# Performance work log

Hardware: AMD Instinct MI355X
Metric: run time of the kernel (lower is better)

The kernel has to match this reference:

```python
import jax, jax.numpy as jnp
import numpy as np

N = 1_000_000
F = 64
G = 8          # num_groups
B = 16         # number of point clouds in batch
EPS = 1e-8


def setup_inputs() -> dict:
    key = jax.random.key(0)
    k1, k2 = jax.random.split(key)
    feats = jax.random.normal(k1, (N, F), dtype=jnp.float32)
    batch_ids = jnp.sort(jax.random.randint(k2, (N,), 0, B))
    gamma = jnp.ones((1, F), dtype=jnp.float32)
    beta = jnp.zeros((1, F), dtype=jnp.float32)
    return {"feats": feats, "batch_ids": batch_ids, "gamma": gamma, "beta": beta}


def reference(feats, batch_ids, gamma, beta):
    gs = F // G  # group_size
    # [N, F] -> [N*gs, G]: each row holds one channel-within-group across all groups
    cur = feats.reshape(-1, G)
    ids = jnp.repeat(batch_ids, gs)  # [N*gs]
    counts = jax.ops.segment_sum(jnp.ones_like(ids, dtype=cur.dtype), ids, num_segments=B)
    counts = jnp.maximum(counts, 1.0)[:, None]                # [B, 1]
    means = jax.ops.segment_sum(cur, ids, num_segments=B) / counts   # [B, G]
    m = means[ids]                                            # [N*gs, G]
    var = jax.ops.segment_sum((cur - m) ** 2, ids, num_segments=B) / counts  # [B, G]
    normed = (cur - m) / jnp.sqrt(var[ids] + EPS)             # [N*gs, G]
    out = normed.reshape(-1, F)
    return out * gamma + beta
```

## Files before the change

### kernel.cpp

```cpp
#include <hip/hip_runtime.h>

#define GN_EPS 1e-8f

static constexpr int F    = 64;
static constexpr int G    = 8;
static constexpr int NB   = 16;
static constexpr int BLK  = 256;
static constexpr int GRID = 2048;

typedef float f32x4 __attribute__((ext_vector_type(4)));

__global__ void gn_prep(const int* __restrict__ ids, int n, int* __restrict__ off,
                        float* __restrict__ zbuf ) {
    const int t = threadIdx.x;
    if (t < 2 * NB * G) zbuf[t] = 0.f;
    if (t < NB + 1) {
        int lo = 0, hi = n;
        while (lo < hi) {
            int mid = (lo + hi) >> 1;
            if (ids[mid] < t) lo = mid + 1; else hi = mid;
        }
        off[t] = lo;
    }
}

__global__ __launch_bounds__(BLK) void gn_stats(
        const float* __restrict__ feats, const int* __restrict__ off_g, int n,
        float* __restrict__ gsum, float* __restrict__ gsq) {
    __shared__ float lsum[NB * G];
    __shared__ float lsq [NB * G];
    __shared__ int   soff[NB + 1];
    const int t = threadIdx.x;
    if (t < NB * G) { lsum[t] = 0.f; lsq[t] = 0.f; }
    if (t < NB + 1) soff[t] = off_g[t];
    __syncthreads();

    const int rpb  = (n + GRID - 1) / GRID;
    const int row0 = (int)blockIdx.x * rpb;
    const int row1 = min(n, row0 + rpb);

    if (row0 < row1) {
        const int quad   = t & 15;
        const int subrow = t >> 4;
        const int lane   = t & 63;
        int b = 0, cur = row0;
        while (cur < row1) {
            while (soff[b + 1] <= cur) ++b;
            const int send = min(row1, soff[b + 1]);
            float s0=0.f,s1=0.f,s2=0.f,s3=0.f,q0=0.f,q1=0.f,q2=0.f,q3=0.f;
            const float* p = feats + (size_t)(cur + subrow) * F + quad * 4;
            int base = cur;
            #pragma unroll 2
            for (; base + 32 <= send; base += 32, p += 32 * F) {
                const float4 x0 = *reinterpret_cast<const float4*>(p);
                const float4 x1 = *reinterpret_cast<const float4*>(p + 16 * F);
                s0 += x0.x; q0 = fmaf(x0.x, x0.x, q0);
                s1 += x0.y; q1 = fmaf(x0.y, x0.y, q1);
                s2 += x0.z; q2 = fmaf(x0.z, x0.z, q2);
                s3 += x0.w; q3 = fmaf(x0.w, x0.w, q3);
                s0 += x1.x; q0 = fmaf(x1.x, x1.x, q0);
                s1 += x1.y; q1 = fmaf(x1.y, x1.y, q1);
                s2 += x1.z; q2 = fmaf(x1.z, x1.z, q2);
                s3 += x1.w; q3 = fmaf(x1.w, x1.w, q3);
            }
            if (base + 16 <= send) {
                const float4 x = *reinterpret_cast<const float4*>(p);
                s0 += x.x; q0 = fmaf(x.x, x.x, q0);
                s1 += x.y; q1 = fmaf(x.y, x.y, q1);
                s2 += x.z; q2 = fmaf(x.z, x.z, q2);
                s3 += x.w; q3 = fmaf(x.w, x.w, q3);
                base += 16; p += 16 * F;
            }
            if (base + subrow < send) {
                const float4 x = *reinterpret_cast<const float4*>(p);
                s0 += x.x; q0 = fmaf(x.x, x.x, q0);
                s1 += x.y; q1 = fmaf(x.y, x.y, q1);
                s2 += x.z; q2 = fmaf(x.z, x.z, q2);
                s3 += x.w; q3 = fmaf(x.w, x.w, q3);
            }
            #pragma unroll
            for (int m = 2; m <= 32; m <<= 1) {
                s0 += __shfl_xor(s0, m); s1 += __shfl_xor(s1, m);
                s2 += __shfl_xor(s2, m); s3 += __shfl_xor(s3, m);
                q0 += __shfl_xor(q0, m); q1 += __shfl_xor(q1, m);
                q2 += __shfl_xor(q2, m); q3 += __shfl_xor(q3, m);
            }
            if (lane < 2) {
                float* ps = &lsum[b * G + lane * 4];
                float* pq = &lsq [b * G + lane * 4];
                atomicAdd(ps + 0, s0); atomicAdd(ps + 1, s1);
                atomicAdd(ps + 2, s2); atomicAdd(ps + 3, s3);
                atomicAdd(pq + 0, q0); atomicAdd(pq + 1, q1);
                atomicAdd(pq + 2, q2); atomicAdd(pq + 3, q3);
            }
            cur = send;
        }
    }
    __syncthreads();
    if (t < NB * G) {
        atomicAdd(&gsum[t], lsum[t]);
        atomicAdd(&gsq [t], lsq [t]);
    }
}

__global__ __launch_bounds__(BLK) void gn_norm(
        const float* __restrict__ feats, const int* __restrict__ off_g, int n,
        const float* __restrict__ gsum, const float* __restrict__ gsq,
        const float* __restrict__ gamma, const float* __restrict__ beta,
        float* __restrict__ out) {
    __shared__ int soff[NB + 1];
    const int t = threadIdx.x;
    if (t < NB + 1) soff[t] = off_g[t];
    __syncthreads();

    const int rpb  = (n + GRID - 1) / GRID;
    const int row0 = (int)blockIdx.x * rpb;
    const int row1 = min(n, row0 + rpb);
    if (row0 >= row1) return;

    const int quad   = t & 15;
    const int subrow = t >> 4;
    const float4 gm = *reinterpret_cast<const float4*>(gamma + quad * 4);
    const float4 bt = *reinterpret_cast<const float4*>(beta  + quad * 4);

    int b = 0, cur = row0;
    while (cur < row1) {
        while (soff[b + 1] <= cur) ++b;
        const int send = min(row1, soff[b + 1]);
        const float4 sm = *reinterpret_cast<const float4*>(gsum + b * G + (quad & 1) * 4);
        const float4 sq = *reinterpret_cast<const float4*>(gsq  + b * G + (quad & 1) * 4);
        const float cnt = (float)max((soff[b + 1] - soff[b]) * (F / G), 1);
        const float rc  = 1.0f / cnt;
        f32x4 a, c;
        {
            const float m0 = sm.x * rc, m1 = sm.y * rc, m2 = sm.z * rc, m3 = sm.w * rc;
            const float v0 = fmaxf(sq.x * rc - m0 * m0, 0.f);
            const float v1 = fmaxf(sq.y * rc - m1 * m1, 0.f);
            const float v2 = fmaxf(sq.z * rc - m2 * m2, 0.f);
            const float v3 = fmaxf(sq.w * rc - m3 * m3, 0.f);
            a.x = gm.x / sqrtf(v0 + GN_EPS); a.y = gm.y / sqrtf(v1 + GN_EPS);
            a.z = gm.z / sqrtf(v2 + GN_EPS); a.w = gm.w / sqrtf(v3 + GN_EPS);
            c.x = fmaf(-m0, a.x, bt.x); c.y = fmaf(-m1, a.y, bt.y);
            c.z = fmaf(-m2, a.z, bt.z); c.w = fmaf(-m3, a.w, bt.w);
        }
        const float* p  = feats + (size_t)(cur + subrow) * F + quad * 4;
        float*       po = out   + (size_t)(cur + subrow) * F + quad * 4;
        int base = cur;
        #pragma unroll 2
        for (; base + 32 <= send; base += 32, p += 32 * F, po += 32 * F) {
            const f32x4 x0 = __builtin_nontemporal_load(reinterpret_cast<const f32x4*>(p));
            const f32x4 x1 = __builtin_nontemporal_load(reinterpret_cast<const f32x4*>(p + 16 * F));
            f32x4 o0, o1;
            o0.x = fmaf(x0.x, a.x, c.x); o0.y = fmaf(x0.y, a.y, c.y);
            o0.z = fmaf(x0.z, a.z, c.z); o0.w = fmaf(x0.w, a.w, c.w);
            o1.x = fmaf(x1.x, a.x, c.x); o1.y = fmaf(x1.y, a.y, c.y);
            o1.z = fmaf(x1.z, a.z, c.z); o1.w = fmaf(x1.w, a.w, c.w);
            __builtin_nontemporal_store(o0, reinterpret_cast<f32x4*>(po));
            __builtin_nontemporal_store(o1, reinterpret_cast<f32x4*>(po + 16 * F));
        }
        if (base + 16 <= send) {
            const f32x4 x = __builtin_nontemporal_load(reinterpret_cast<const f32x4*>(p));
            f32x4 o;
            o.x = fmaf(x.x, a.x, c.x); o.y = fmaf(x.y, a.y, c.y);
            o.z = fmaf(x.z, a.z, c.z); o.w = fmaf(x.w, a.w, c.w);
            __builtin_nontemporal_store(o, reinterpret_cast<f32x4*>(po));
            base += 16; p += 16 * F; po += 16 * F;
        }
        if (base + subrow < send) {
            const f32x4 x = __builtin_nontemporal_load(reinterpret_cast<const f32x4*>(p));
            f32x4 o;
            o.x = fmaf(x.x, a.x, c.x); o.y = fmaf(x.y, a.y, c.y);
            o.z = fmaf(x.z, a.z, c.z); o.w = fmaf(x.w, a.w, c.w);
            __builtin_nontemporal_store(o, reinterpret_cast<f32x4*>(po));
        }
        cur = send;
    }
}

extern "C" void kernel_launch(void* const* d_in, const int* in_sizes, int n_in,
                              void* d_out, int out_size, void* d_ws, size_t ws_size,
                              hipStream_t stream) {
    const float* feats = (const float*)d_in[0];
    const int*   ids   = (const int*)  d_in[1];
    const float* gamma = (const float*)d_in[2];
    const float* beta  = (const float*)d_in[3];
    const int n = in_sizes[1];

    float* gsum = (float*)d_ws;
    float* gsq  = gsum + NB * G;
    int*   off  = (int*)(gsq + NB * G);

    gn_prep <<<1, BLK, 0, stream>>>(ids, n, off, gsum);
    gn_stats<<<GRID, BLK, 0, stream>>>(feats, off, n, gsum, gsq);
    gn_norm <<<GRID, BLK, 0, stream>>>(feats, off, n, gsum, gsq, gamma, beta, (float*)d_out);
}
```

Measured before the change: 156.5 us.

## Spread stats atomics over slots and traverse norm rows in reverse order

```diff
diff --git a/kernel.cpp b/kernel.cpp
--- a/kernel.cpp
+++ b/kernel.cpp
@@ -2,18 +2,20 @@
 
 #define GN_EPS 1e-8f
 
-static constexpr int F    = 64;
-static constexpr int G    = 8;
-static constexpr int NB   = 16;
-static constexpr int BLK  = 256;
-static constexpr int GRID = 2048;
+static constexpr int F     = 64;
+static constexpr int G     = 8;
+static constexpr int NB    = 16;
+static constexpr int BLK   = 256;
+static constexpr int GRID  = 2048;
+static constexpr int NSLOT = 16;
 
 typedef float f32x4 __attribute__((ext_vector_type(4)));
+
 
 __global__ void gn_prep(const int* __restrict__ ids, int n, int* __restrict__ off,
                         float* __restrict__ zbuf ) {
     const int t = threadIdx.x;
-    if (t < 2 * NB * G) zbuf[t] = 0.f;
+    for (int i = t; i < 2 * NSLOT * NB * G; i += BLK) zbuf[i] = 0.f;
     if (t < NB + 1) {
         int lo = 0, hi = n;
         while (lo < hi) {
@@ -50,10 +52,11 @@
             float s0=0.f,s1=0.f,s2=0.f,s3=0.f,q0=0.f,q1=0.f,q2=0.f,q3=0.f;
             const float* p = feats + (size_t)(cur + subrow) * F + quad * 4;
             int base = cur;
-            #pragma unroll 2
-            for (; base + 32 <= send; base += 32, p += 32 * F) {
+            for (; base + 64 <= send; base += 64, p += 64 * F) {
                 const float4 x0 = *reinterpret_cast<const float4*>(p);
                 const float4 x1 = *reinterpret_cast<const float4*>(p + 16 * F);
+                const float4 x2 = *reinterpret_cast<const float4*>(p + 32 * F);
+                const float4 x3 = *reinterpret_cast<const float4*>(p + 48 * F);
                 s0 += x0.x; q0 = fmaf(x0.x, x0.x, q0);
                 s1 += x0.y; q1 = fmaf(x0.y, x0.y, q1);
                 s2 += x0.z; q2 = fmaf(x0.z, x0.z, q2);
@@ -62,14 +65,21 @@
                 s1 += x1.y; q1 = fmaf(x1.y, x1.y, q1);
                 s2 += x1.z; q2 = fmaf(x1.z, x1.z, q2);
                 s3 += x1.w; q3 = fmaf(x1.w, x1.w, q3);
-            }
-            if (base + 16 <= send) {
+                s0 += x2.x; q0 = fmaf(x2.x, x2.x, q0);
+                s1 += x2.y; q1 = fmaf(x2.y, x2.y, q1);
+                s2 += x2.z; q2 = fmaf(x2.z, x2.z, q2);
+                s3 += x2.w; q3 = fmaf(x2.w, x2.w, q3);
+                s0 += x3.x; q0 = fmaf(x3.x, x3.x, q0);
+                s1 += x3.y; q1 = fmaf(x3.y, x3.y, q1);
+                s2 += x3.z; q2 = fmaf(x3.z, x3.z, q2);
+                s3 += x3.w; q3 = fmaf(x3.w, x3.w, q3);
+            }
+            for (; base + 16 <= send; base += 16, p += 16 * F) {
                 const float4 x = *reinterpret_cast<const float4*>(p);
                 s0 += x.x; q0 = fmaf(x.x, x.x, q0);
                 s1 += x.y; q1 = fmaf(x.y, x.y, q1);
                 s2 += x.z; q2 = fmaf(x.z, x.z, q2);
                 s3 += x.w; q3 = fmaf(x.w, x.w, q3);
-                base += 16; p += 16 * F;
             }
             if (base + subrow < send) {
                 const float4 x = *reinterpret_cast<const float4*>(p);
@@ -98,8 +108,9 @@
     }
     __syncthreads();
     if (t < NB * G) {
-        atomicAdd(&gsum[t], lsum[t]);
-        atomicAdd(&gsq [t], lsq [t]);
+        const int slot = (int)blockIdx.x & (NSLOT - 1);
+        atomicAdd(&gsum[slot * NB * G + t], lsum[t]);
+        atomicAdd(&gsq [slot * NB * G + t], lsq [t]);
     }
 }
 
@@ -123,12 +134,16 @@
     const float4 gm = *reinterpret_cast<const float4*>(gamma + quad * 4);
     const float4 bt = *reinterpret_cast<const float4*>(beta  + quad * 4);
 
-    int b = 0, cur = row0;
-    while (cur < row1) {
-        while (soff[b + 1] <= cur) ++b;
-        const int send = min(row1, soff[b + 1]);
-        const float4 sm = *reinterpret_cast<const float4*>(gsum + b * G + (quad & 1) * 4);
-        const float4 sq = *reinterpret_cast<const float4*>(gsq  + b * G + (quad & 1) * 4);
+    int b = NB - 1, e = row1;
+    while (e > row0) {
+        while (soff[b] >= e) --b;
+        const int sstart = max(row0, soff[b]);
+        f32x4 sm = {0.f, 0.f, 0.f, 0.f}, sq = {0.f, 0.f, 0.f, 0.f};
+        #pragma unroll
+        for (int k = 0; k < NSLOT; ++k) {
+            sm += *reinterpret_cast<const f32x4*>(gsum + k * NB * G + b * G + (quad & 1) * 4);
+            sq += *reinterpret_cast<const f32x4*>(gsq  + k * NB * G + b * G + (quad & 1) * 4);
+        }
         const float cnt = (float)max((soff[b + 1] - soff[b]) * (F / G), 1);
         const float rc  = 1.0f / cnt;
         f32x4 a, c;
@@ -143,37 +158,47 @@
             c.x = fmaf(-m0, a.x, bt.x); c.y = fmaf(-m1, a.y, bt.y);
             c.z = fmaf(-m2, a.z, bt.z); c.w = fmaf(-m3, a.w, bt.w);
         }
-        const float* p  = feats + (size_t)(cur + subrow) * F + quad * 4;
-        float*       po = out   + (size_t)(cur + subrow) * F + quad * 4;
-        int base = cur;
-        #pragma unroll 2
-        for (; base + 32 <= send; base += 32, p += 32 * F, po += 32 * F) {
+        int hi = e;
+        for (; hi - sstart >= 64; hi -= 64) {
+            const float* p  = feats + (size_t)(hi - 64 + subrow) * F + quad * 4;
+            float*       po = out   + (size_t)(hi - 64 + subrow) * F + quad * 4;
             const f32x4 x0 = __builtin_nontemporal_load(reinterpret_cast<const f32x4*>(p));
             const f32x4 x1 = __builtin_nontemporal_load(reinterpret_cast<const f32x4*>(p + 16 * F));
-            f32x4 o0, o1;
+            const f32x4 x2 = __builtin_nontemporal_load(reinterpret_cast<const f32x4*>(p + 32 * F));
+            const f32x4 x3 = __builtin_nontemporal_load(reinterpret_cast<const f32x4*>(p + 48 * F));
+            f32x4 o0, o1, o2, o3;
             o0.x = fmaf(x0.x, a.x, c.x); o0.y = fmaf(x0.y, a.y, c.y);
             o0.z = fmaf(x0.z, a.z, c.z); o0.w = fmaf(x0.w, a.w, c.w);
             o1.x = fmaf(x1.x, a.x, c.x); o1.y = fmaf(x1.y, a.y, c.y);
             o1.z = fmaf(x1.z, a.z, c.z); o1.w = fmaf(x1.w, a.w, c.w);
+            o2.x = fmaf(x2.x, a.x, c.x); o2.y = fmaf(x2.y, a.y, c.y);
+            o2.z = fmaf(x2.z, a.z, c.z); o2.w = fmaf(x2.w, a.w, c.w);
+            o3.x = fmaf(x3.x, a.x, c.x); o3.y = fmaf(x3.y, a.y, c.y);
+            o3.z = fmaf(x3.z, a.z, c.z); o3.w = fmaf(x3.w, a.w, c.w);
             __builtin_nontemporal_store(o0, reinterpret_cast<f32x4*>(po));
             __builtin_nontemporal_store(o1, reinterpret_cast<f32x4*>(po + 16 * F));
-        }
-        if (base + 16 <= send) {
+            __builtin_nontemporal_store(o2, reinterpret_cast<f32x4*>(po + 32 * F));
+            __builtin_nontemporal_store(o3, reinterpret_cast<f32x4*>(po + 48 * F));
+        }
+        for (; hi - sstart >= 16; hi -= 16) {
+            const float* p  = feats + (size_t)(hi - 16 + subrow) * F + quad * 4;
+            float*       po = out   + (size_t)(hi - 16 + subrow) * F + quad * 4;
             const f32x4 x = __builtin_nontemporal_load(reinterpret_cast<const f32x4*>(p));
             f32x4 o;
             o.x = fmaf(x.x, a.x, c.x); o.y = fmaf(x.y, a.y, c.y);
             o.z = fmaf(x.z, a.z, c.z); o.w = fmaf(x.w, a.w, c.w);
             __builtin_nontemporal_store(o, reinterpret_cast<f32x4*>(po));
-            base += 16; p += 16 * F; po += 16 * F;
-        }
-        if (base + subrow < send) {
+        }
+        if (sstart + subrow < hi) {
+            const float* p  = feats + (size_t)(sstart + subrow) * F + quad * 4;
+            float*       po = out   + (size_t)(sstart + subrow) * F + quad * 4;
             const f32x4 x = __builtin_nontemporal_load(reinterpret_cast<const f32x4*>(p));
             f32x4 o;
             o.x = fmaf(x.x, a.x, c.x); o.y = fmaf(x.y, a.y, c.y);
             o.z = fmaf(x.z, a.z, c.z); o.w = fmaf(x.w, a.w, c.w);
             __builtin_nontemporal_store(o, reinterpret_cast<f32x4*>(po));
         }
-        cur = send;
+        e = sstart;
     }
 }
 
@@ -187,8 +212,8 @@
     const int n = in_sizes[1];
 
     float* gsum = (float*)d_ws;
-    float* gsq  = gsum + NB * G;
-    int*   off  = (int*)(gsq + NB * G);
+    float* gsq  = gsum + NSLOT * NB * G;
+    int*   off  = (int*)(gsq + NSLOT * NB * G);
 
     gn_prep <<<1, BLK, 0, stream>>>(ids, n, off, gsum);
     gn_stats<<<GRID, BLK, 0, stream>>>(feats, off, n, gsum, gsq);
```

Result: faster. 132.5 us (-15.3%).
